# Performance work log

Measured on AMD Instinct MI355X. Metric: run time of the kernel, lower is better.

## Reference

```python
import jax, jax.numpy as jnp
import numpy as np

N = 262144   # number of occupied voxels (sparse points)
C = 64       # channels
G = 128
K = 27       # 3x3x3 kernel offsets


def _build_kernel_map(rng):
    # Unique occupied voxel coordinates on a G^3 grid.
    flat = rng.choice(G ** 3, size=N, replace=False)
    order = np.argsort(flat)
    skeys = flat[order]
    coords = np.stack(np.unravel_index(flat, (G, G, G)), axis=1).astype(np.int64)  # [N,3]
    offsets = np.array([[dx, dy, dz] for dx in (-1, 0, 1) for dy in (-1, 0, 1) for dz in (-1, 0, 1)], np.int64)
    nb = np.full((N, K), -1, np.int32)  # -1 == no neighbor at this offset
    for k in range(K):
        nc = coords + offsets[k]
        valid = np.all((nc >= 0) & (nc < G), axis=1)
        nkey = (nc[:, 0] * G + nc[:, 1]) * G + nc[:, 2]
        pos = np.clip(np.searchsorted(skeys, nkey), 0, N - 1)
        hit = valid & (skeys[pos] == nkey)
        nb[hit, k] = order[pos[hit]].astype(np.int32)
    return nb


def setup_inputs() -> dict:
    nb = _build_kernel_map(np.random.default_rng(0))
    key = jax.random.key(0)
    k1, k2, k3, k4, k5 = jax.random.split(key, 5)
    feat = jax.random.normal(k1, (N, C), jnp.float32)
    W = jax.random.normal(k2, (C, C), jnp.float32) / np.float32(np.sqrt(C))   # 1x1 bottleneck weight
    b1 = jax.random.normal(k3, (C,), jnp.float32) * 0.01                      # bottleneck bias
    dw = jax.random.normal(k4, (K, C), jnp.float32) / np.float32(np.sqrt(K))  # channelwise 3^3 kernel
    b2 = jax.random.normal(k5, (C,), jnp.float32) * 0.01                      # channelwise bias
    return {"feat": feat, "neighbor_idx": jnp.asarray(nb), "W": W, "b1": b1, "b2": b2, "dw": dw}


def reference(feat, neighbor_idx, W, b1, b2, dw):
    # bottleneck: 1x1 sparse conv == pointwise linear over features
    bx = feat @ W + b1  # [N,C]
    mask = neighbor_idx >= 0
    safe = jnp.where(mask, neighbor_idx, 0)
    # channelwise (depthwise) 3x3x3 sparse conv: sum over 27 offsets of
    # gathered neighbor features times per-channel weight. scan over the
    # fixed 27 offsets to avoid a [N,27,C] intermediate.
    def body(acc, inp):
        wk, idxk, mk = inp  # [C], [N], [N]
        g = jnp.where(mk[:, None], bx[idxk], 0.0)
        return acc + g * wk, None
    acc, _ = jax.lax.scan(body, jnp.zeros_like(bx), (dw, safe.T, mask.T))
    # residual add (note: the module never applies its ReLU in forward)
    return feat + acc + b2
```

## Files before the change

kernel.cpp:

```cpp
#include <hip/hip_runtime.h>
#include <hip/hip_bf16.h>

#define NPTS 262144
#define NC 64
#define NK 27
#define RPB 128
#define NBS 132

typedef __attribute__((ext_vector_type(8))) short bf16x8;
typedef __attribute__((ext_vector_type(4))) float f32x4;
typedef __attribute__((ext_vector_type(2))) float f32x2;

__device__ __forceinline__ unsigned cvtpk(float lo, float hi) {
    unsigned r;
    asm("v_cvt_pk_bf16_f32 %0, %1, %2" : "=v"(r) : "v"(lo), "v"(hi));
    return r;
}
__device__ __forceinline__ f32x2 up2(unsigned u) {
    f32x2 r;
    r.x = __uint_as_float(u << 16);
    r.y = __uint_as_float(u & 0xffff0000u);
    return r;
}

union BF { unsigned u[4]; bf16x8 v; };


__global__ __launch_bounds__(256) void gemm_mfma(const float* __restrict__ feat,
                                                 const float* __restrict__ W,
                                                 const float* __restrict__ b1,
                                                 ushort* __restrict__ bx,
                                                 uint* __restrict__ zrow) {
    __shared__ float Ws[NC * NC];
    __shared__ float b1S[NC];
    int t = threadIdx.x;
    if (zrow && blockIdx.x == 0 && t < 32) zrow[t] = 0u;
#pragma unroll
    for (int i = 0; i < 4; ++i)
        ((float4*)Ws)[t + i * 256] = ((const float4*)W)[t + i * 256];
    if (t < NC) b1S[t] = b1[t];
    __syncthreads();

    int lane = t & 63;
    int col = lane & 15;
    int kg = lane >> 4;
    int wid = blockIdx.x * 4 + (t >> 6);
    const int NWAVES = 2048 * 4;
    const int NTILES = NPTS / 16;

    BF Bf[2][4];
#pragma unroll
    for (int ks = 0; ks < 2; ++ks)
#pragma unroll
        for (int ct = 0; ct < 4; ++ct)
#pragma unroll
            for (int r = 0; r < 4; ++r) {
                float lo = Ws[(ks * 32 + kg * 8 + 2 * r) * NC + ct * 16 + col];
                float hi = Ws[(ks * 32 + kg * 8 + 2 * r + 1) * NC + ct * 16 + col];
                Bf[ks][ct].u[r] = cvtpk(lo, hi);
            }
    float bias[4];
#pragma unroll
    for (int ct = 0; ct < 4; ++ct) bias[ct] = b1S[ct * 16 + col];

    for (int tile = wid; tile < NTILES; tile += NWAVES) {
        long r0 = (long)tile * 16;
        const float* ap = feat + (r0 + col) * NC + kg * 8;
        float4 a0 = *(const float4*)(ap);
        float4 a1 = *(const float4*)(ap + 4);
        float4 a2 = *(const float4*)(ap + 32);
        float4 a3 = *(const float4*)(ap + 36);
        BF A0, A1;
        A0.u[0] = cvtpk(a0.x, a0.y); A0.u[1] = cvtpk(a0.z, a0.w);
        A0.u[2] = cvtpk(a1.x, a1.y); A0.u[3] = cvtpk(a1.z, a1.w);
        A1.u[0] = cvtpk(a2.x, a2.y); A1.u[1] = cvtpk(a2.z, a2.w);
        A1.u[2] = cvtpk(a3.x, a3.y); A1.u[3] = cvtpk(a3.z, a3.w);

        f32x4 acc[4];
#pragma unroll
        for (int ct = 0; ct < 4; ++ct) {
            acc[ct] = (f32x4){bias[ct], bias[ct], bias[ct], bias[ct]};
            acc[ct] = __builtin_amdgcn_mfma_f32_16x16x32_bf16(A0.v, Bf[0][ct].v, acc[ct], 0, 0, 0);
            acc[ct] = __builtin_amdgcn_mfma_f32_16x16x32_bf16(A1.v, Bf[1][ct].v, acc[ct], 0, 0, 0);
        }
#pragma unroll
        for (int i = 0; i < 4; ++i) {
            uint* bu = (uint*)(bx + (r0 + kg * 4 + i) * NC);
            bu[col]      = cvtpk(acc[0][i], acc[1][i]);
            bu[16 + col] = cvtpk(acc[2][i], acc[3][i]);
        }
    }
}

template <bool SENT>
__global__ __launch_bounds__(256, 5) void dwconv(const float* __restrict__ feat,
                                                 const int* __restrict__ nb,
                                                 const float* __restrict__ b2,
                                                 const float* __restrict__ dw,
                                                 const ushort* __restrict__ bx,
                                                 float* __restrict__ out) {
    __shared__ int nbT[NK * NBS];
    __shared__ float dwS[NK * NC];
    __shared__ float b2S[NC];
    int t = threadIdx.x;
    for (int i = t; i < NK * NC; i += 256) {
        int p = i & 63;
        int ch = ((p >> 1) & 15) + ((p & 1) << 4) + (p & 32);
        dwS[i] = dw[(i & ~63) + ch];
    }
    if (t < NC) b2S[t] = b2[t];

    int b = blockIdx.x;
    int chunk = gridDim.x >> 3;
    int sb = (b & 7) * chunk + (b >> 3);

    const int* nsrc = nb + (size_t)sb * RPB * NK;
    for (int i = t; i < RPB * NK; i += 256) {
        int r = i / NK;
        int k = i - r * NK;
        int v = nsrc[i];
        if (SENT) v = (v < 0) ? NPTS : v;
        nbT[k * NBS + r] = v;
    }
    __syncthreads();

    int g = t >> 3;
    int q = t & 7;
    long row0 = (long)sb * RPB + g * 4;
    unsigned qo = (unsigned)q << 4;

    f32x2 acc[4][4];
#pragma unroll
    for (int j = 0; j < 4; ++j)
#pragma unroll
        for (int i = 0; i < 4; ++i) acc[j][i] = (f32x2){0.f, 0.f};

    const char* bp = (const char*)bx;
    const int* nbase = nbT + g * 4;
    const f32x2* wbase = (const f32x2*)dwS + q * 4;

#pragma unroll 3
    for (int k = 0; k < NK; ++k) {
        int4 idx = *(const int4*)(nbase + k * NBS);
        int sx = idx.x, sy = idx.y, sz = idx.z, sw = idx.w;
        if (!SENT) { sx = max(sx, 0); sy = max(sy, 0); sz = max(sz, 0); sw = max(sw, 0); }
        uint4 g0 = *(const uint4*)(bp + (((unsigned)sx << 7) + qo));
        uint4 g1 = *(const uint4*)(bp + (((unsigned)sy << 7) + qo));
        uint4 g2 = *(const uint4*)(bp + (((unsigned)sz << 7) + qo));
        uint4 g3 = *(const uint4*)(bp + (((unsigned)sw << 7) + qo));
        if (!SENT) {
            unsigned m0 = idx.x >= 0 ? 0xffffffffu : 0u;
            unsigned m1 = idx.y >= 0 ? 0xffffffffu : 0u;
            unsigned m2 = idx.z >= 0 ? 0xffffffffu : 0u;
            unsigned m3 = idx.w >= 0 ? 0xffffffffu : 0u;
            g0.x &= m0; g0.y &= m0; g0.z &= m0; g0.w &= m0;
            g1.x &= m1; g1.y &= m1; g1.z &= m1; g1.w &= m1;
            g2.x &= m2; g2.y &= m2; g2.z &= m2; g2.w &= m2;
            g3.x &= m3; g3.y &= m3; g3.z &= m3; g3.w &= m3;
        }
        f32x2 w0 = wbase[k * 32 + 0];
        f32x2 w1 = wbase[k * 32 + 1];
        f32x2 w2 = wbase[k * 32 + 2];
        f32x2 w3 = wbase[k * 32 + 3];
        acc[0][0] += up2(g0.x) * w0; acc[0][1] += up2(g0.y) * w1;
        acc[0][2] += up2(g0.z) * w2; acc[0][3] += up2(g0.w) * w3;
        acc[1][0] += up2(g1.x) * w0; acc[1][1] += up2(g1.y) * w1;
        acc[1][2] += up2(g1.z) * w2; acc[1][3] += up2(g1.w) * w3;
        acc[2][0] += up2(g2.x) * w0; acc[2][1] += up2(g2.y) * w1;
        acc[2][2] += up2(g2.z) * w2; acc[2][3] += up2(g2.w) * w3;
        acc[3][0] += up2(g3.x) * w0; acc[3][1] += up2(g3.y) * w1;
        acc[3][2] += up2(g3.z) * w2; acc[3][3] += up2(g3.w) * w3;
    }

    int lo_c0 = (q < 4) ? 4 * q : 16 + 4 * q;
    int hi_c0 = lo_c0 + 16;
#pragma unroll
    for (int j = 0; j < 4; ++j) {
        long row = row0 + j;
        const float* fp = feat + row * NC;
        float4 flo = *(const float4*)(fp + lo_c0);
        float4 fhi = *(const float4*)(fp + hi_c0);
        float4 olo = make_float4(acc[j][0].x + flo.x + b2S[lo_c0 + 0],
                                 acc[j][1].x + flo.y + b2S[lo_c0 + 1],
                                 acc[j][2].x + flo.z + b2S[lo_c0 + 2],
                                 acc[j][3].x + flo.w + b2S[lo_c0 + 3]);
        float4 ohi = make_float4(acc[j][0].y + fhi.x + b2S[hi_c0 + 0],
                                 acc[j][1].y + fhi.y + b2S[hi_c0 + 1],
                                 acc[j][2].y + fhi.z + b2S[hi_c0 + 2],
                                 acc[j][3].y + fhi.w + b2S[hi_c0 + 3]);
        *(float4*)(out + row * NC + lo_c0) = olo;
        *(float4*)(out + row * NC + hi_c0) = ohi;
    }
}

extern "C" void kernel_launch(void* const* d_in, const int* in_sizes, int n_in,
                              void* d_out, int out_size, void* d_ws, size_t ws_size,
                              hipStream_t stream) {
    const float* feat = (const float*)d_in[0];
    const int*   nb   = (const int*)d_in[1];
    const float* W    = (const float*)d_in[2];
    const float* b1   = (const float*)d_in[3];
    const float* b2   = (const float*)d_in[4];
    const float* dw   = (const float*)d_in[5];
    float* out = (float*)d_out;
    ushort* bx = (ushort*)d_ws;

    bool sent = ws_size >= (size_t)(NPTS + 1) * NC * sizeof(ushort);
    uint* zrow = sent ? (uint*)(bx + (size_t)NPTS * NC) : nullptr;

    gemm_mfma<<<2048, 256, 0, stream>>>(feat, W, b1, bx, zrow);
    if (sent)
        dwconv<true><<<NPTS / RPB, 256, 0, stream>>>(feat, nb, b2, dw, bx, out);
    else
        dwconv<false><<<NPTS / RPB, 256, 0, stream>>>(feat, nb, b2, dw, bx, out);
}
```

Measured before the change: 204.8 us.

## Shrink dwconv blocks to 32 rows with one row per thread group

The depthwise conv kernel now gives each 8-thread group one row instead of four, so each block covers 32 rows and the grid has four times as many blocks. The neighbor table is stored row-major in shared memory with a padded stride, and the sentinel path double-buffers the gathers across offsets. Launch bounds rise to 8 blocks per CU. The aim is higher occupancy and a smaller shared-memory footprint to hide gather latency, at the cost of less memory-level parallelism per thread (one gather in flight instead of four) and more per-block setup, since the 27x64 weights are reloaded by four times as many blocks.

```diff
diff --git a/kernel.cpp b/kernel.cpp
--- a/kernel.cpp
+++ b/kernel.cpp
@@ -4,8 +4,7 @@
 #define NPTS 262144
 #define NC 64
 #define NK 27
-#define RPB 128
-#define NBS 132
+#define NBS2 28
 
 typedef __attribute__((ext_vector_type(8))) short bf16x8;
 typedef __attribute__((ext_vector_type(4))) float f32x4;
@@ -92,16 +91,15 @@
     }
 }
 
-template <bool SENT>
-__global__ __launch_bounds__(256, 5) void dwconv(const float* __restrict__ feat,
-                                                 const int* __restrict__ nb,
-                                                 const float* __restrict__ b2,
-                                                 const float* __restrict__ dw,
-                                                 const ushort* __restrict__ bx,
-                                                 float* __restrict__ out) {
-    __shared__ int nbT[NK * NBS];
+__global__ __launch_bounds__(256, 8) void dwconv_s(const float* __restrict__ feat,
+                                                   const int* __restrict__ nb,
+                                                   const float* __restrict__ b2,
+                                                   const float* __restrict__ dw,
+                                                   const ushort* __restrict__ bx,
+                                                   float* __restrict__ out) {
     __shared__ float dwS[NK * NC];
     __shared__ float b2S[NC];
+    __shared__ int nbS[32 * NBS2];
     int t = threadIdx.x;
     for (int i = t; i < NK * NC; i += 256) {
         int p = i & 63;
@@ -114,83 +112,136 @@
     int chunk = gridDim.x >> 3;
     int sb = (b & 7) * chunk + (b >> 3);
 
-    const int* nsrc = nb + (size_t)sb * RPB * NK;
-    for (int i = t; i < RPB * NK; i += 256) {
+    const int* nsrc = nb + (size_t)sb * 32 * NK;
+    for (int i = t; i < 32 * NK; i += 256) {
         int r = i / NK;
         int k = i - r * NK;
         int v = nsrc[i];
-        if (SENT) v = (v < 0) ? NPTS : v;
-        nbT[k * NBS + r] = v;
+        nbS[r * NBS2 + k] = (v < 0) ? NPTS : v;
     }
     __syncthreads();
 
-    int g = t >> 3;
+    int r = t >> 3;
     int q = t & 7;
-    long row0 = (long)sb * RPB + g * 4;
+    long row = (long)sb * 32 + r;
     unsigned qo = (unsigned)q << 4;
 
-    f32x2 acc[4][4];
-#pragma unroll
-    for (int j = 0; j < 4; ++j)
-#pragma unroll
-        for (int i = 0; i < 4; ++i) acc[j][i] = (f32x2){0.f, 0.f};
-
     const char* bp = (const char*)bx;
-    const int* nbase = nbT + g * 4;
-    const f32x2* wbase = (const f32x2*)dwS + q * 4;
-
-#pragma unroll 3
-    for (int k = 0; k < NK; ++k) {
-        int4 idx = *(const int4*)(nbase + k * NBS);
-        int sx = idx.x, sy = idx.y, sz = idx.z, sw = idx.w;
-        if (!SENT) { sx = max(sx, 0); sy = max(sy, 0); sz = max(sz, 0); sw = max(sw, 0); }
-        uint4 g0 = *(const uint4*)(bp + (((unsigned)sx << 7) + qo));
-        uint4 g1 = *(const uint4*)(bp + (((unsigned)sy << 7) + qo));
-        uint4 g2 = *(const uint4*)(bp + (((unsigned)sz << 7) + qo));
-        uint4 g3 = *(const uint4*)(bp + (((unsigned)sw << 7) + qo));
-        if (!SENT) {
-            unsigned m0 = idx.x >= 0 ? 0xffffffffu : 0u;
-            unsigned m1 = idx.y >= 0 ? 0xffffffffu : 0u;
-            unsigned m2 = idx.z >= 0 ? 0xffffffffu : 0u;
-            unsigned m3 = idx.w >= 0 ? 0xffffffffu : 0u;
-            g0.x &= m0; g0.y &= m0; g0.z &= m0; g0.w &= m0;
-            g1.x &= m1; g1.y &= m1; g1.z &= m1; g1.w &= m1;
-            g2.x &= m2; g2.y &= m2; g2.z &= m2; g2.w &= m2;
-            g3.x &= m3; g3.y &= m3; g3.z &= m3; g3.w &= m3;
-        }
-        f32x2 w0 = wbase[k * 32 + 0];
-        f32x2 w1 = wbase[k * 32 + 1];
-        f32x2 w2 = wbase[k * 32 + 2];
-        f32x2 w3 = wbase[k * 32 + 3];
-        acc[0][0] += up2(g0.x) * w0; acc[0][1] += up2(g0.y) * w1;
-        acc[0][2] += up2(g0.z) * w2; acc[0][3] += up2(g0.w) * w3;
-        acc[1][0] += up2(g1.x) * w0; acc[1][1] += up2(g1.y) * w1;
-        acc[1][2] += up2(g1.z) * w2; acc[1][3] += up2(g1.w) * w3;
-        acc[2][0] += up2(g2.x) * w0; acc[2][1] += up2(g2.y) * w1;
-        acc[2][2] += up2(g2.z) * w2; acc[2][3] += up2(g2.w) * w3;
-        acc[3][0] += up2(g3.x) * w0; acc[3][1] += up2(g3.y) * w1;
-        acc[3][2] += up2(g3.z) * w2; acc[3][3] += up2(g3.w) * w3;
-    }
+    const int* nrow = nbS + r * NBS2;
+    const f32x4* wq = (const f32x4*)dwS + q * 2;
+
+    f32x2 acc0 = {0,0}, acc1 = {0,0}, acc2 = {0,0}, acc3 = {0,0};
+
+#define GATHER(d, ii) d = *(const uint4*)(bp + (((unsigned)(ii) << 7) + qo))
+#define CONSUME(gg, kk)                                                  \
+    {                                                                    \
+        f32x4 wa = wq[(kk) * 16];                                        \
+        f32x4 wb = wq[(kk) * 16 + 1];                                    \
+        acc0 += up2(gg.x) * (f32x2){wa.x, wa.y};                         \
+        acc1 += up2(gg.y) * (f32x2){wa.z, wa.w};                         \
+        acc2 += up2(gg.z) * (f32x2){wb.x, wb.y};                         \
+        acc3 += up2(gg.w) * (f32x2){wb.z, wb.w};                         \
+    }
+
+    int iA = nrow[0], iB;
+    uint4 ga, gb;
+    GATHER(ga, iA);
+
+#pragma unroll
+    for (int k = 0; k < NK - 1; k += 2) {
+        iB = nrow[k + 1];
+        GATHER(gb, iB);
+        CONSUME(ga, k);
+        iA = nrow[k + 2];
+        GATHER(ga, iA);
+        CONSUME(gb, k + 1);
+    }
+    CONSUME(ga, NK - 1);
+#undef GATHER
+#undef CONSUME
 
     int lo_c0 = (q < 4) ? 4 * q : 16 + 4 * q;
     int hi_c0 = lo_c0 + 16;
-#pragma unroll
-    for (int j = 0; j < 4; ++j) {
-        long row = row0 + j;
-        const float* fp = feat + row * NC;
-        float4 flo = *(const float4*)(fp + lo_c0);
-        float4 fhi = *(const float4*)(fp + hi_c0);
-        float4 olo = make_float4(acc[j][0].x + flo.x + b2S[lo_c0 + 0],
-                                 acc[j][1].x + flo.y + b2S[lo_c0 + 1],
-                                 acc[j][2].x + flo.z + b2S[lo_c0 + 2],
-                                 acc[j][3].x + flo.w + b2S[lo_c0 + 3]);
-        float4 ohi = make_float4(acc[j][0].y + fhi.x + b2S[hi_c0 + 0],
-                                 acc[j][1].y + fhi.y + b2S[hi_c0 + 1],
-                                 acc[j][2].y + fhi.z + b2S[hi_c0 + 2],
-                                 acc[j][3].y + fhi.w + b2S[hi_c0 + 3]);
-        *(float4*)(out + row * NC + lo_c0) = olo;
-        *(float4*)(out + row * NC + hi_c0) = ohi;
-    }
+    const float* fp = feat + row * NC;
+    float4 flo = *(const float4*)(fp + lo_c0);
+    float4 fhi = *(const float4*)(fp + hi_c0);
+    float4 olo = make_float4(acc0.x + flo.x + b2S[lo_c0 + 0],
+                             acc1.x + flo.y + b2S[lo_c0 + 1],
+                             acc2.x + flo.z + b2S[lo_c0 + 2],
+                             acc3.x + flo.w + b2S[lo_c0 + 3]);
+    float4 ohi = make_float4(acc0.y + fhi.x + b2S[hi_c0 + 0],
+                             acc1.y + fhi.y + b2S[hi_c0 + 1],
+                             acc2.y + fhi.z + b2S[hi_c0 + 2],
+                             acc3.y + fhi.w + b2S[hi_c0 + 3]);
+    *(float4*)(out + row * NC + lo_c0) = olo;
+    *(float4*)(out + row * NC + hi_c0) = ohi;
+}
+
+__global__ __launch_bounds__(256, 8) void dwconv_f(const float* __restrict__ feat,
+                                                   const int* __restrict__ nb,
+                                                   const float* __restrict__ b2,
+                                                   const float* __restrict__ dw,
+                                                   const ushort* __restrict__ bx,
+                                                   float* __restrict__ out) {
+    __shared__ float dwS[NK * NC];
+    __shared__ float b2S[NC];
+    __shared__ int nbS[32 * NBS2];
+    int t = threadIdx.x;
+    for (int i = t; i < NK * NC; i += 256) {
+        int p = i & 63;
+        int ch = ((p >> 1) & 15) + ((p & 1) << 4) + (p & 32);
+        dwS[i] = dw[(i & ~63) + ch];
+    }
+    if (t < NC) b2S[t] = b2[t];
+    int b = blockIdx.x;
+    int chunk = gridDim.x >> 3;
+    int sb = (b & 7) * chunk + (b >> 3);
+    const int* nsrc = nb + (size_t)sb * 32 * NK;
+    for (int i = t; i < 32 * NK; i += 256) {
+        int r = i / NK;
+        int k = i - r * NK;
+        nbS[r * NBS2 + k] = nsrc[i];
+    }
+    __syncthreads();
+
+    int r = t >> 3, q = t & 7;
+    long row = (long)sb * 32 + r;
+    unsigned qo = (unsigned)q << 4;
+    const char* bp = (const char*)bx;
+    const int* nrow = nbS + r * NBS2;
+    const f32x4* wq = (const f32x4*)dwS + q * 2;
+    f32x2 acc0 = {0,0}, acc1 = {0,0}, acc2 = {0,0}, acc3 = {0,0};
+
+#pragma unroll
+    for (int k = 0; k < NK; ++k) {
+        int id = nrow[k];
+        int ids = max(id, 0);
+        uint4 g = *(const uint4*)(bp + (((unsigned)ids << 7) + qo));
+        unsigned m = id >= 0 ? 0xffffffffu : 0u;
+        g.x &= m; g.y &= m; g.z &= m; g.w &= m;
+        f32x4 wa = wq[k * 16];
+        f32x4 wb = wq[k * 16 + 1];
+        acc0 += up2(g.x) * (f32x2){wa.x, wa.y};
+        acc1 += up2(g.y) * (f32x2){wa.z, wa.w};
+        acc2 += up2(g.z) * (f32x2){wb.x, wb.y};
+        acc3 += up2(g.w) * (f32x2){wb.z, wb.w};
+    }
+
+    int lo_c0 = (q < 4) ? 4 * q : 16 + 4 * q;
+    int hi_c0 = lo_c0 + 16;
+    const float* fp = feat + row * NC;
+    float4 flo = *(const float4*)(fp + lo_c0);
+    float4 fhi = *(const float4*)(fp + hi_c0);
+    float4 olo = make_float4(acc0.x + flo.x + b2S[lo_c0 + 0],
+                             acc1.x + flo.y + b2S[lo_c0 + 1],
+                             acc2.x + flo.z + b2S[lo_c0 + 2],
+                             acc3.x + flo.w + b2S[lo_c0 + 3]);
+    float4 ohi = make_float4(acc0.y + fhi.x + b2S[hi_c0 + 0],
+                             acc1.y + fhi.y + b2S[hi_c0 + 1],
+                             acc2.y + fhi.z + b2S[hi_c0 + 2],
+                             acc3.y + fhi.w + b2S[hi_c0 + 3]);
+    *(float4*)(out + row * NC + lo_c0) = olo;
+    *(float4*)(out + row * NC + hi_c0) = ohi;
 }
 
 extern "C" void kernel_launch(void* const* d_in, const int* in_sizes, int n_in,
@@ -210,7 +261,7 @@
 
     gemm_mfma<<<2048, 256, 0, stream>>>(feat, W, b1, bx, zrow);
     if (sent)
-        dwconv<true><<<NPTS / RPB, 256, 0, stream>>>(feat, nb, b2, dw, bx, out);
+        dwconv_s<<<NPTS / 32, 256, 0, stream>>>(feat, nb, b2, dw, bx, out);
     else
-        dwconv<false><<<NPTS / RPB, 256, 0, stream>>>(feat, nb, b2, dw, bx, out);
-}
+        dwconv_f<<<NPTS / 32, 256, 0, stream>>>(feat, nb, b2, dw, bx, out);
+}
```

Result: no change. 204.9 us (+0.0%).
